# Kernel tuning notes

Measured on AMD Instinct MI355X. Metric: run time of the kernel, lower is better.

The kernel has to match this reference:

```python
import jax, jax.numpy as jnp
import numpy as np

H = 4096          # hidden_size
I = 11008         # intermediate_size
G = 128           # AWQ group_size
# AWQ interleaved nibble order within each packed int32
_ORDER = jnp.array([0, 4, 1, 5, 2, 6, 3, 7], dtype=jnp.int32) * 4


def _mk_lin(key, K, N):
    k1, k2, k3 = jax.random.split(key, 3)
    qw = jax.random.randint(k1, (K, N // 8), 0, 100, dtype=jnp.int32)
    qz = jax.random.randint(k2, (K // G, N // 8), 0, 100, dtype=jnp.int32)
    sc = jax.random.normal(k3, (K // G, N), dtype=jnp.float32) * 0.02
    return qw, qz, sc


def setup_inputs() -> dict:
    key = jax.random.key(0)
    ks = jax.random.split(key, 7)
    x = jax.random.normal(ks[0], (8, 16, H), dtype=jnp.float32)
    ln1_w = jnp.ones((H,), dtype=jnp.float32)
    ln2_w = jnp.ones((H,), dtype=jnp.float32)
    qkv_qw, qkv_qz, qkv_sc = _mk_lin(ks[1], H, 3 * H)
    o_qw, o_qz, o_sc = _mk_lin(ks[2], H, H)
    gu_qw, gu_qz, gu_sc = _mk_lin(ks[3], H, 2 * I)
    dn_qw, dn_qz, dn_sc = _mk_lin(ks[4], I, H)
    return dict(x=x, ln1_w=ln1_w, ln2_w=ln2_w,
                qkv_qw=qkv_qw, qkv_qz=qkv_qz, qkv_sc=qkv_sc,
                o_qw=o_qw, o_qz=o_qz, o_sc=o_sc,
                gu_qw=gu_qw, gu_qz=gu_qz, gu_sc=gu_sc,
                dn_qw=dn_qw, dn_qz=dn_qz, dn_sc=dn_sc)


def rmsnorm(x, w, eps=1e-6):
    return x * jax.lax.rsqrt(jnp.mean(x * x, axis=-1, keepdims=True) + eps) * w


def dequant(qw, qz, sc):
    # qw: [K, N//8] int32 -> [K, N]; qz: [K//G, N//8] -> [K//G, N]
    K = qw.shape[0]
    N = sc.shape[1]
    w = ((qw[:, :, None] >> _ORDER) & 0xF).reshape(K, N).astype(sc.dtype)
    z = ((qz[:, :, None] >> _ORDER) & 0xF).reshape(K // G, N).astype(sc.dtype)
    return (w - jnp.repeat(z, G, axis=0)) * jnp.repeat(sc, G, axis=0)


def lite_linear(x, qw, qz, sc):
    return x @ dequant(qw, qz, sc)


def reference(x, ln1_w, ln2_w,
              qkv_qw, qkv_qz, qkv_sc,
              o_qw, o_qz, o_sc,
              gu_qw, gu_qz, gu_sc,
              dn_qw, dn_qz, dn_sc):
    residual = x
    h = rmsnorm(x, ln1_w)
    h = lite_linear(h, qkv_qw, qkv_qz, qkv_sc)[..., :H]  # mock attn: take q slice
    h = lite_linear(h, o_qw, o_qz, o_sc)
    h = residual + h
    residual = h
    h = rmsnorm(h, ln2_w)
    gate_up = lite_linear(h, gu_qw, gu_qz, gu_sc)
    gate, up = gate_up[..., :I], gate_up[..., I:]
    h = lite_linear(jax.nn.silu(gate) * up, dn_qw, dn_qz, dn_sc)
    return residual + h
```

## Files before the change

kernel.cpp:

```cpp
#include <hip/hip_runtime.h>

typedef unsigned int   u32;
typedef unsigned short u16;

typedef _Float16 h2  __attribute__((ext_vector_type(2)));
typedef _Float16 h8  __attribute__((ext_vector_type(8)));
typedef float    f32x4 __attribute__((ext_vector_type(4)));

#define M_TOK 128

__device__ __forceinline__ u16 f2h_(float f) {
    _Float16 h = (_Float16)f; return __builtin_bit_cast(u16, h);
}
__device__ __forceinline__ float h2f_(u16 b) {
    _Float16 h = __builtin_bit_cast(_Float16, b); return (float)h;
}
__device__ __forceinline__ void acc8(uint4 v, float* s) {
#pragma unroll
    for (int i = 0; i < 4; ++i) {
        u32 w = ((const u32*)&v)[i];
        s[2 * i]     += h2f_((u16)(w & 0xFFFF));
        s[2 * i + 1] += h2f_((u16)(w >> 16));
    }
}

__constant__ int SHC[8] = {0, 16, 4, 20, 8, 24, 12, 28};

__launch_bounds__(256)
__global__ void pack_zs(const int* __restrict__ qz, const float* __restrict__ sc,
                        u32* __restrict__ zs, int qws, int scs, int Ncols, int total) {
    const int idx = blockIdx.x * 256 + threadIdx.x;
    if (idx >= total) return;
    const int g = idx / Ncols, n = idx - g * Ncols;
    const u32 d = (u32)qz[(size_t)g * qws + (n >> 3)];
    const u32 zj = (d >> SHC[n & 7]) & 15u;
    const u32 mz = 0xE400u | zj;
    const u16 sh = f2h_(sc[(size_t)g * scs + n]);
    zs[(size_t)g * Ncols + n] = mz | ((u32)sh << 16);
}


__launch_bounds__(256)
__global__ void rmsnorm_k(const float* __restrict__ in, const float* __restrict__ w,
                          u16* __restrict__ out) {
    const int row = blockIdx.x;
    const float* x = in + (size_t)row * 4096;
    float ss = 0.f;
#pragma unroll
    for (int j = 0; j < 16; ++j) {
        float v = x[threadIdx.x + 256 * j];
        ss += v * v;
    }
#pragma unroll
    for (int off = 32; off > 0; off >>= 1) ss += __shfl_down(ss, off, 64);
    __shared__ float ws4[4];
    if ((threadIdx.x & 63) == 0) ws4[threadIdx.x >> 6] = ss;
    __syncthreads();
    float total = ws4[0] + ws4[1] + ws4[2] + ws4[3];
    float r = rsqrtf(total * (1.f / 4096.f) + 1e-6f);
    const int mt = row >> 4, l16 = row & 15;
#pragma unroll
    for (int c2 = 0; c2 < 2; ++c2) {
        int c = threadIdx.x * 2 + c2;
        int kb = c >> 2, qq = c & 3;
        u16 o8[8];
#pragma unroll
        for (int j = 0; j < 8; ++j) {
            int i = c * 8 + j;
            o8[j] = f2h_(x[i] * r * w[i]);
        }
        *(uint4*)(out + ((size_t)(kb * 8 + mt) * 64 + qq * 16 + l16) * 8) = *(const uint4*)o8;
    }
}

__launch_bounds__(256, 2)
__global__ void gemm_awq(const u16* __restrict__ A, const u32* __restrict__ zs,
                         const int* __restrict__ qw, u16* __restrict__ part,
                         int qws, int N, int K, int kchunk) {
    __shared__ __align__(16) char ldsB[4 * 4608];

    const int tid = threadIdx.x, w = tid >> 6, lane = tid & 63;
    const int q = lane >> 4, l16 = lane & 15;
    const int n0w = blockIdx.x * 128 + w * 32;
    const int pc0 = n0w >> 3;
    const int kp = lane & 31, h = lane >> 5;
    const int sk = blockIdx.y, kc0 = sk * kchunk, kend = min(kc0 + kchunk, K);

    char* myB   = ldsB + w * 4608;
    char* wbase = myB + kp * 4;
    const u16* Ala = A + lane * 8;
    const int* qws_base = qw + pc0;
    const u32* zsA = zs + n0w + h * 8;
    const u32* zsB = zs + n0w + 16 + h * 8;

    f32x4 acc[8][2] = {};
    uint4 za0, za1, zb0, zb1;

    auto ldraw = [&](int k0) -> uint4 {
        return *(const uint4*)(qws_base + (size_t)(k0 + lane) * qws);
    };
    auto loadzs = [&](int g) {
        za0 = *(const uint4*)(zsA + (size_t)g * N);
        za1 = *(const uint4*)(zsA + (size_t)g * N + 4);
        zb0 = *(const uint4*)(zsB + (size_t)g * N);
        zb1 = *(const uint4*)(zsB + (size_t)g * N + 4);
    };
    auto route = [&](uint4 rv, u32* d) {
        const int i0 = kp * 8, i1 = i0 + 4;
        int b00 = __builtin_amdgcn_ds_bpermute(i0, (int)rv.x);
        int b10 = __builtin_amdgcn_ds_bpermute(i0, (int)rv.y);
        int b20 = __builtin_amdgcn_ds_bpermute(i0, (int)rv.z);
        int b30 = __builtin_amdgcn_ds_bpermute(i0, (int)rv.w);
        int b01 = __builtin_amdgcn_ds_bpermute(i1, (int)rv.x);
        int b11 = __builtin_amdgcn_ds_bpermute(i1, (int)rv.y);
        int b21 = __builtin_amdgcn_ds_bpermute(i1, (int)rv.z);
        int b31 = __builtin_amdgcn_ds_bpermute(i1, (int)rv.w);
        d[0] = (u32)(h ? b10 : b00);
        d[1] = (u32)(h ? b11 : b01);
        d[2] = (u32)(h ? b30 : b20);
        d[3] = (u32)(h ? b31 : b21);
    };
    auto emit8 = [&](u32 w0, u32 w1, int nb, uint4 z0, uint4 z1) {
        char* bb = wbase + nb * 144;
        u32 w0s = w0 >> 4, w1s = w1 >> 4;
        auto em = [&](int j, u32 a0, u32 a1, int b, u32 zsj) {
            h2 mz = __builtin_bit_cast(h2, __builtin_amdgcn_perm(zsj, zsj, 0x01000100u));
            h2 s2 = __builtin_bit_cast(h2, __builtin_amdgcn_perm(zsj, zsj, 0x03020302u));
            u32 t = __builtin_amdgcn_perm(a1, a0, (u32)(b | ((b + 4) << 16)));
            u32 u = (t & 0x000F000Fu) | 0x64006400u;
            h2 v = (__builtin_bit_cast(h2, u) + mz) * s2;
            *(u32*)(bb + j * 144) = __builtin_bit_cast(u32, v);
        };
        em(0, w0, w1, 0, z0.x);  em(4, w0, w1, 1, z1.x);
        em(1, w0, w1, 2, z0.y);  em(5, w0, w1, 3, z1.y);
        em(2, w0s, w1s, 0, z0.z); em(6, w0s, w1s, 1, z1.z);
        em(3, w0s, w1s, 2, z0.w); em(7, w0s, w1s, 3, z1.w);
    };
    auto lda = [&](int k, uint4(&dst)[2][8]) {
        const int kb = k >> 5;
#pragma unroll
        for (int c = 0; c < 2; ++c)
#pragma unroll
            for (int mt = 0; mt < 8; ++mt)
                dst[c][mt] = *(const uint4*)(Ala + (size_t)((kb + c) * 8 + mt) * 512);
    };

    uint4 afA[2][8], afB[2][8];
    uint4 rv_n = {0,0,0,0};

    loadzs(kc0 >> 7);
    uint4 rv0 = ldraw(kc0);
    if (kc0 + 64 < kend) rv_n = ldraw(kc0 + 64);
    lda(kc0, afA);
    {
        u32 qd[4];
        route(rv0, qd);
        emit8(qd[0], qd[1], h * 8, za0, za1);
        emit8(qd[2], qd[3], 16 + h * 8, zb0, zb1);
    }
    if (((kc0 + 64) & 127) == 0 && kc0 + 64 < kend)
        loadzs((kc0 + 64) >> 7);

    auto step = [&](int k0, uint4(&cur)[2][8], uint4(&nxt)[2][8]) {
        const bool kn1 = (k0 + 64) < kend, kn2 = (k0 + 128) < kend;
        if (kn1) lda(k0 + 64, nxt);
        uint4 bv[2][2];
#pragma unroll
        for (int c = 0; c < 2; ++c)
#pragma unroll
            for (int nt = 0; nt < 2; ++nt)
                bv[c][nt] = *(const uint4*)(myB + (nt * 16 + l16) * 144 + c * 64 + q * 16);
        uint4 rv_f = {0,0,0,0};
        if (kn2) rv_f = ldraw(k0 + 128);
        if (kn1) {
            u32 qd[4];
            route(rv_n, qd);
            emit8(qd[0], qd[1], h * 8, za0, za1);
            emit8(qd[2], qd[3], 16 + h * 8, zb0, zb1);
        }
        if (kn2 && (((k0 + 128) & 127) == 0))
            loadzs((k0 + 128) >> 7);
#pragma unroll
        for (int c = 0; c < 2; ++c)
#pragma unroll
            for (int mt = 0; mt < 8; ++mt)
#pragma unroll
                for (int nt = 0; nt < 2; ++nt)
                    acc[mt][nt] = __builtin_amdgcn_mfma_f32_16x16x32_f16(
                        __builtin_bit_cast(h8, cur[c][mt]),
                        __builtin_bit_cast(h8, bv[c][nt]),
                        acc[mt][nt], 0, 0, 0);
        rv_n = rv_f;
    };
    for (int k0 = kc0; k0 < kend; k0 += 128) {
        step(k0, afA, afB);
        if (k0 + 64 < kend) step(k0 + 64, afB, afA);
    }

    u16* pp = part + (size_t)sk * M_TOK * N;
#pragma unroll
    for (int mt = 0; mt < 8; ++mt)
#pragma unroll
        for (int nt = 0; nt < 2; ++nt) {
            const int n = n0w + nt * 16 + l16;
#pragma unroll
            for (int r = 0; r < 4; ++r) {
                const int m = mt * 16 + q * 4 + r;
                pp[(size_t)m * N + n] = f2h_(acc[mt][nt][r]);
            }
        }
}

__launch_bounds__(256)
__global__ void reduce_to_afrag(const u16* __restrict__ part, u16* __restrict__ out,
                                int SK) {
    const int idx = blockIdx.x * 256 + threadIdx.x;
    const int m = idx >> 9, c = idx & 511;
    float s[8] = {};
    for (int k = 0; k < SK; ++k)
        acc8(*(const uint4*)(part + (size_t)k * 524288 + (size_t)m * 4096 + c * 8), s);
    const int kb = c >> 2, qq = c & 3, mt = m >> 4, l16 = m & 15;
    u16 o8[8];
#pragma unroll
    for (int j = 0; j < 8; ++j) o8[j] = f2h_(s[j]);
    *(uint4*)(out + ((size_t)(kb * 8 + mt) * 64 + qq * 16 + l16) * 8) = *(const uint4*)o8;
}

__launch_bounds__(256)
__global__ void reduce_add_f32(const u16* __restrict__ part, const float* __restrict__ resin,
                               float* __restrict__ out, int SK) {
    const int idx = blockIdx.x * 256 + threadIdx.x;
    const size_t base = (size_t)idx * 8;
    float s[8];
    *(float4*)&s[0] = *(const float4*)(resin + base);
    *(float4*)&s[4] = *(const float4*)(resin + base + 4);
    for (int k = 0; k < SK; ++k)
        acc8(*(const uint4*)(part + (size_t)k * 524288 + base), s);
    *(float4*)(out + base)     = *(const float4*)&s[0];
    *(float4*)(out + base + 4) = *(const float4*)&s[4];
}

__launch_bounds__(256)
__global__ void silu_mul(const u16* __restrict__ part, u16* __restrict__ act) {
    const int idx = blockIdx.x * 256 + threadIdx.x;
    const int m = idx / 1376, c = idx - m * 1376;
    const int nb = c * 8;
    float g[8] = {}, u[8] = {};
    for (int k = 0; k < 3; ++k) {
        const size_t base = (size_t)k * 2818048 + (size_t)m * 22016 + nb;
        acc8(*(const uint4*)(part + base), g);
        acc8(*(const uint4*)(part + base + 11008), u);
    }
    const int kb = nb >> 5, qq = (nb >> 3) & 3, mt = m >> 4, l16 = m & 15;
    u16 o8[8];
#pragma unroll
    for (int j = 0; j < 8; ++j) {
        float a = g[j] / (1.f + __expf(-g[j])) * u[j];
        o8[j] = f2h_(a);
    }
    *(uint4*)(act + ((size_t)(kb * 8 + mt) * 64 + qq * 16 + l16) * 8) = *(const uint4*)o8;
}

extern "C" void kernel_launch(void* const* d_in, const int* in_sizes, int n_in,
                              void* d_out, int out_size, void* d_ws, size_t ws_size,
                              hipStream_t stream) {
    const float* x      = (const float*)d_in[0];
    const float* ln1_w  = (const float*)d_in[1];
    const float* ln2_w  = (const float*)d_in[2];
    const int*   qkv_qw = (const int*)d_in[3];
    const int*   qkv_qz = (const int*)d_in[4];
    const float* qkv_sc = (const float*)d_in[5];
    const int*   o_qw   = (const int*)d_in[6];
    const int*   o_qz   = (const int*)d_in[7];
    const float* o_sc   = (const float*)d_in[8];
    const int*   gu_qw  = (const int*)d_in[9];
    const int*   gu_qz  = (const int*)d_in[10];
    const float* gu_sc  = (const float*)d_in[11];
    const int*   dn_qw  = (const int*)d_in[12];
    const int*   dn_qz  = (const int*)d_in[13];
    const float* dn_sc  = (const float*)d_in[14];
    float* out = (float*)d_out;

    char* ws = (char*)d_ws;
    u16*   pbuf = (u16*)(ws);
    u32*   zsb  = (u32*)(ws + 16908288);
    u16*   act  = (u16*)(ws + 19726336);
    float* res2 = (float*)(ws + 22544384);
    u16*   slot = (u16*)(ws + 24641536);

    rmsnorm_k<<<128, 256, 0, stream>>>(x, ln1_w, slot);
    pack_zs<<<512, 256, 0, stream>>>(qkv_qz, qkv_sc, zsb, 1536, 12288, 4096, 131072);

    gemm_awq<<<dim3(32, 16), 256, 0, stream>>>(slot, zsb, qkv_qw, pbuf,
                                               1536, 4096, 4096, 256);
    reduce_to_afrag<<<256, 256, 0, stream>>>(pbuf, slot, 16);
    pack_zs<<<512, 256, 0, stream>>>(o_qz, o_sc, zsb, 512, 4096, 4096, 131072);

    gemm_awq<<<dim3(32, 16), 256, 0, stream>>>(slot, zsb, o_qw, pbuf,
                                               512, 4096, 4096, 256);
    reduce_add_f32<<<256, 256, 0, stream>>>(pbuf, x, res2, 16);

    rmsnorm_k<<<128, 256, 0, stream>>>(res2, ln2_w, slot);
    pack_zs<<<2752, 256, 0, stream>>>(gu_qz, gu_sc, zsb, 2752, 22016, 22016, 704512);

    gemm_awq<<<dim3(172, 3), 256, 0, stream>>>(slot, zsb, gu_qw, pbuf,
                                               2752, 22016, 4096, 1408);
    silu_mul<<<688, 256, 0, stream>>>(pbuf, act);
    pack_zs<<<1376, 256, 0, stream>>>(dn_qz, dn_sc, zsb, 512, 4096, 4096, 352256);

    gemm_awq<<<dim3(32, 16), 256, 0, stream>>>(act, zsb, dn_qw, pbuf,
                                               512, 4096, 11008, 704);
    reduce_add_f32<<<256, 256, 0, stream>>>(pbuf, res2, out, 16);
}
```

Baseline: 304.0 us.

## Halve per-wave N tile in AWQ GEMM and drop A double-buffering for occupancy

Each wave now covers 16 output columns instead of 32, so it loads and dequantizes half as many packed weights and keeps eight accumulators instead of sixteen. The A-fragment double buffer is replaced by loads issued inside each 64-K step, and launch bounds rise to four blocks per SIMD with doubled grid width. The aim is more waves in flight to hide memory latency on this weight-bandwidth-bound GEMM. In exchange, A fragments are reloaded twice as often across blocks, and A-load latency is no longer prefetched a step ahead.

Result: slower. 343.6 us (+13.0%).

```diff
diff --git a/kernel.cpp b/kernel.cpp
--- a/kernel.cpp
+++ b/kernel.cpp
@@ -73,55 +73,46 @@
     }
 }
 
-__launch_bounds__(256, 2)
+__launch_bounds__(256, 4)
 __global__ void gemm_awq(const u16* __restrict__ A, const u32* __restrict__ zs,
                          const int* __restrict__ qw, u16* __restrict__ part,
                          int qws, int N, int K, int kchunk) {
-    __shared__ __align__(16) char ldsB[4 * 4608];
+    __shared__ __align__(16) char ldsB[4 * 2304];
 
     const int tid = threadIdx.x, w = tid >> 6, lane = tid & 63;
     const int q = lane >> 4, l16 = lane & 15;
-    const int n0w = blockIdx.x * 128 + w * 32;
+    const int n0w = blockIdx.x * 64 + w * 16;
     const int pc0 = n0w >> 3;
     const int kp = lane & 31, h = lane >> 5;
     const int sk = blockIdx.y, kc0 = sk * kchunk, kend = min(kc0 + kchunk, K);
 
-    char* myB   = ldsB + w * 4608;
+    char* myB   = ldsB + w * 2304;
     char* wbase = myB + kp * 4;
     const u16* Ala = A + lane * 8;
     const int* qws_base = qw + pc0;
-    const u32* zsA = zs + n0w + h * 8;
-    const u32* zsB = zs + n0w + 16 + h * 8;
-
-    f32x4 acc[8][2] = {};
-    uint4 za0, za1, zb0, zb1;
-
-    auto ldraw = [&](int k0) -> uint4 {
-        return *(const uint4*)(qws_base + (size_t)(k0 + lane) * qws);
+    const u32* zsO = zs + n0w + h * 8;
+
+    f32x4 acc[8] = {};
+    uint4 za0, za1;
+
+    auto ldraw = [&](int k0) -> uint2 {
+        return *(const uint2*)(qws_base + (size_t)(k0 + lane) * qws);
     };
     auto loadzs = [&](int g) {
-        za0 = *(const uint4*)(zsA + (size_t)g * N);
-        za1 = *(const uint4*)(zsA + (size_t)g * N + 4);
-        zb0 = *(const uint4*)(zsB + (size_t)g * N);
-        zb1 = *(const uint4*)(zsB + (size_t)g * N + 4);
-    };
-    auto route = [&](uint4 rv, u32* d) {
+        za0 = *(const uint4*)(zsO + (size_t)g * N);
+        za1 = *(const uint4*)(zsO + (size_t)g * N + 4);
+    };
+    auto route = [&](uint2 rv, u32& w0, u32& w1) {
         const int i0 = kp * 8, i1 = i0 + 4;
         int b00 = __builtin_amdgcn_ds_bpermute(i0, (int)rv.x);
+        int b01 = __builtin_amdgcn_ds_bpermute(i1, (int)rv.x);
         int b10 = __builtin_amdgcn_ds_bpermute(i0, (int)rv.y);
-        int b20 = __builtin_amdgcn_ds_bpermute(i0, (int)rv.z);
-        int b30 = __builtin_amdgcn_ds_bpermute(i0, (int)rv.w);
-        int b01 = __builtin_amdgcn_ds_bpermute(i1, (int)rv.x);
         int b11 = __builtin_amdgcn_ds_bpermute(i1, (int)rv.y);
-        int b21 = __builtin_amdgcn_ds_bpermute(i1, (int)rv.z);
-        int b31 = __builtin_amdgcn_ds_bpermute(i1, (int)rv.w);
-        d[0] = (u32)(h ? b10 : b00);
-        d[1] = (u32)(h ? b11 : b01);
-        d[2] = (u32)(h ? b30 : b20);
-        d[3] = (u32)(h ? b31 : b21);
-    };
-    auto emit8 = [&](u32 w0, u32 w1, int nb, uint4 z0, uint4 z1) {
-        char* bb = wbase + nb * 144;
+        w0 = (u32)(h ? b10 : b00);
+        w1 = (u32)(h ? b11 : b01);
+    };
+    auto emit8 = [&](u32 w0, u32 w1, uint4 z0, uint4 z1) {
+        char* bb = wbase + (h * 8) * 144;
         u32 w0s = w0 >> 4, w1s = w1 >> 4;
         auto em = [&](int j, u32 a0, u32 a1, int b, u32 zsj) {
             h2 mz = __builtin_bit_cast(h2, __builtin_amdgcn_perm(zsj, zsj, 0x01000100u));
@@ -136,78 +127,63 @@
         em(2, w0s, w1s, 0, z0.z); em(6, w0s, w1s, 1, z1.z);
         em(3, w0s, w1s, 2, z0.w); em(7, w0s, w1s, 3, z1.w);
     };
-    auto lda = [&](int k, uint4(&dst)[2][8]) {
-        const int kb = k >> 5;
-#pragma unroll
-        for (int c = 0; c < 2; ++c)
-#pragma unroll
-            for (int mt = 0; mt < 8; ++mt)
-                dst[c][mt] = *(const uint4*)(Ala + (size_t)((kb + c) * 8 + mt) * 512);
-    };
-
-    uint4 afA[2][8], afB[2][8];
-    uint4 rv_n = {0,0,0,0};
+
+    uint2 rv_n = {0, 0};
 
     loadzs(kc0 >> 7);
-    uint4 rv0 = ldraw(kc0);
+    uint2 rv0 = ldraw(kc0);
     if (kc0 + 64 < kend) rv_n = ldraw(kc0 + 64);
-    lda(kc0, afA);
     {
-        u32 qd[4];
-        route(rv0, qd);
-        emit8(qd[0], qd[1], h * 8, za0, za1);
-        emit8(qd[2], qd[3], 16 + h * 8, zb0, zb1);
+        u32 w0, w1;
+        route(rv0, w0, w1);
+        emit8(w0, w1, za0, za1);
     }
     if (((kc0 + 64) & 127) == 0 && kc0 + 64 < kend)
         loadzs((kc0 + 64) >> 7);
 
-    auto step = [&](int k0, uint4(&cur)[2][8], uint4(&nxt)[2][8]) {
+    for (int k0 = kc0; k0 < kend; k0 += 64) {
         const bool kn1 = (k0 + 64) < kend, kn2 = (k0 + 128) < kend;
-        if (kn1) lda(k0 + 64, nxt);
-        uint4 bv[2][2];
-#pragma unroll
-        for (int c = 0; c < 2; ++c)
-#pragma unroll
-            for (int nt = 0; nt < 2; ++nt)
-                bv[c][nt] = *(const uint4*)(myB + (nt * 16 + l16) * 144 + c * 64 + q * 16);
-        uint4 rv_f = {0,0,0,0};
+        const int kb0 = k0 >> 5;
+        uint4 bv0 = *(const uint4*)(myB + l16 * 144 + q * 16);
+        uint4 bv1 = *(const uint4*)(myB + l16 * 144 + 64 + q * 16);
+        uint4 af0[8];
+#pragma unroll
+        for (int mt = 0; mt < 8; ++mt)
+            af0[mt] = *(const uint4*)(Ala + (size_t)(kb0 * 8 + mt) * 512);
+        uint2 rv_f = {0, 0};
         if (kn2) rv_f = ldraw(k0 + 128);
         if (kn1) {
-            u32 qd[4];
-            route(rv_n, qd);
-            emit8(qd[0], qd[1], h * 8, za0, za1);
-            emit8(qd[2], qd[3], 16 + h * 8, zb0, zb1);
+            u32 w0, w1;
+            route(rv_n, w0, w1);
+            emit8(w0, w1, za0, za1);
         }
         if (kn2 && (((k0 + 128) & 127) == 0))
             loadzs((k0 + 128) >> 7);
 #pragma unroll
-        for (int c = 0; c < 2; ++c)
-#pragma unroll
-            for (int mt = 0; mt < 8; ++mt)
-#pragma unroll
-                for (int nt = 0; nt < 2; ++nt)
-                    acc[mt][nt] = __builtin_amdgcn_mfma_f32_16x16x32_f16(
-                        __builtin_bit_cast(h8, cur[c][mt]),
-                        __builtin_bit_cast(h8, bv[c][nt]),
-                        acc[mt][nt], 0, 0, 0);
+        for (int mt = 0; mt < 8; ++mt)
+            acc[mt] = __builtin_amdgcn_mfma_f32_16x16x32_f16(
+                __builtin_bit_cast(h8, af0[mt]), __builtin_bit_cast(h8, bv0),
+                acc[mt], 0, 0, 0);
+        uint4 af1[8];
+#pragma unroll
+        for (int mt = 0; mt < 8; ++mt)
+            af1[mt] = *(const uint4*)(Ala + (size_t)((kb0 + 1) * 8 + mt) * 512);
+#pragma unroll
+        for (int mt = 0; mt < 8; ++mt)
+            acc[mt] = __builtin_amdgcn_mfma_f32_16x16x32_f16(
+                __builtin_bit_cast(h8, af1[mt]), __builtin_bit_cast(h8, bv1),
+                acc[mt], 0, 0, 0);
         rv_n = rv_f;
-    };
-    for (int k0 = kc0; k0 < kend; k0 += 128) {
-        step(k0, afA, afB);
-        if (k0 + 64 < kend) step(k0 + 64, afB, afA);
     }
 
     u16* pp = part + (size_t)sk * M_TOK * N;
+    const int n = n0w + l16;
 #pragma unroll
     for (int mt = 0; mt < 8; ++mt)
 #pragma unroll
-        for (int nt = 0; nt < 2; ++nt) {
-            const int n = n0w + nt * 16 + l16;
-#pragma unroll
-            for (int r = 0; r < 4; ++r) {
-                const int m = mt * 16 + q * 4 + r;
-                pp[(size_t)m * N + n] = f2h_(acc[mt][nt][r]);
-            }
+        for (int r = 0; r < 4; ++r) {
+            const int m = mt * 16 + q * 4 + r;
+            pp[(size_t)m * N + n] = f2h_(acc[mt][r]);
         }
 }
 
@@ -291,24 +267,24 @@
     rmsnorm_k<<<128, 256, 0, stream>>>(x, ln1_w, slot);
     pack_zs<<<512, 256, 0, stream>>>(qkv_qz, qkv_sc, zsb, 1536, 12288, 4096, 131072);
 
-    gemm_awq<<<dim3(32, 16), 256, 0, stream>>>(slot, zsb, qkv_qw, pbuf,
+    gemm_awq<<<dim3(64, 16), 256, 0, stream>>>(slot, zsb, qkv_qw, pbuf,
                                                1536, 4096, 4096, 256);
     reduce_to_afrag<<<256, 256, 0, stream>>>(pbuf, slot, 16);
     pack_zs<<<512, 256, 0, stream>>>(o_qz, o_sc, zsb, 512, 4096, 4096, 131072);
 
-    gemm_awq<<<dim3(32, 16), 256, 0, stream>>>(slot, zsb, o_qw, pbuf,
+    gemm_awq<<<dim3(64, 16), 256, 0, stream>>>(slot, zsb, o_qw, pbuf,
                                                512, 4096, 4096, 256);
     reduce_add_f32<<<256, 256, 0, stream>>>(pbuf, x, res2, 16);
 
     rmsnorm_k<<<128, 256, 0, stream>>>(res2, ln2_w, slot);
     pack_zs<<<2752, 256, 0, stream>>>(gu_qz, gu_sc, zsb, 2752, 22016, 22016, 704512);
 
-    gemm_awq<<<dim3(172, 3), 256, 0, stream>>>(slot, zsb, gu_qw, pbuf,
+    gemm_awq<<<dim3(344, 3), 256, 0, stream>>>(slot, zsb, gu_qw, pbuf,
                                                2752, 22016, 4096, 1408);
     silu_mul<<<688, 256, 0, stream>>>(pbuf, act);
     pack_zs<<<1376, 256, 0, stream>>>(dn_qz, dn_sc, zsb, 512, 4096, 4096, 352256);
 
-    gemm_awq<<<dim3(32, 16), 256, 0, stream>>>(act, zsb, dn_qw, pbuf,
+    gemm_awq<<<dim3(64, 16), 256, 0, stream>>>(act, zsb, dn_qw, pbuf,
                                                512, 4096, 11008, 704);
     reduce_add_f32<<<256, 256, 0, stream>>>(pbuf, res2, out, 16);
 }
```
